# Performance work log

Measured on AMD Instinct MI355X. Metric: run time of the kernel, lower is better.

The kernel has to match this reference:

```python
import jax, jax.numpy as jnp
import numpy as np

NEG_INF = -1000000000.0


def _masked_softmax_scores(a, b, mask):
    # a: [B,H,S,D], b: [B,H,S,D] -> probs [B,H,S,S]
    d = a.shape[-1]
    scores = jnp.einsum('bhqd,bhkd->bhqk', a, b) / jnp.sqrt(jnp.asarray(d, a.dtype))
    scores = jnp.where(mask == 0, jnp.asarray(NEG_INF, scores.dtype), scores)
    return jax.nn.softmax(scores, axis=-1)


def setup_inputs() -> dict:
    key = jax.random.key(0)
    ks = jax.random.split(key, 8)
    B, H, S, D = 8, 12, 512, 64
    return {
        'query': jax.random.normal(ks[0], (B, H, S, D), dtype=jnp.float32),
        'key': jax.random.normal(ks[1], (B, H, S, D), dtype=jnp.float32),
        'value': jax.random.normal(ks[2], (B, H, S, D), dtype=jnp.float32),
        'mask': jax.random.randint(ks[3], (B, 1, S, S), 0, 2, dtype=jnp.int32),
        'x_original1': jax.random.normal(ks[4], (B, H, S, D), dtype=jnp.float32),
        'x_original2': jax.random.normal(ks[5], (B, H, S, D), dtype=jnp.float32),
        'x_position1': jax.random.normal(ks[6], (B, H, S, D), dtype=jnp.float32),
        'x_position2': jax.random.normal(ks[7], (B, H, S, D), dtype=jnp.float32),
    }


def reference(query, key, value, mask, x_original1, x_original2, x_position1, x_position2):
    p_attn = _masked_softmax_scores(query, key, mask)
    p_attn_ww = _masked_softmax_scores(x_original1, x_original2, mask)
    p_attn_wp = _masked_softmax_scores(x_original1, x_position2, mask)
    p_attn_pw = _masked_softmax_scores(x_position1, x_original2, mask)
    p_attn_pp = _masked_softmax_scores(x_position1, x_position2, mask)
    out = jnp.einsum('bhqk,bhkd->bhqd', p_attn, value)
    return (out, p_attn, p_attn_ww, p_attn_wp, p_attn_pw, p_attn_pp)
```

## Files before the change

### kernel.cpp

```cpp
#include <hip/hip_runtime.h>
#include <hip/hip_bf16.h>

typedef _Float16 f16;
typedef f16 f16x2 __attribute__((ext_vector_type(2)));
typedef f16 f16x4 __attribute__((ext_vector_type(4)));
typedef f16 f16x8 __attribute__((ext_vector_type(8)));
typedef float f32x4 __attribute__((ext_vector_type(4)));
typedef float f32x16 __attribute__((ext_vector_type(16)));
typedef int i32x4 __attribute__((ext_vector_type(4)));
typedef unsigned char u8;
typedef u8 u8x4 __attribute__((ext_vector_type(4)));

#define SEQ 512
#define DIM 64
#define NBH 96
#define OUT0 3145728
#define PSZ  25165824
#define MSZ  262144

__device__ __forceinline__ int swz(int row, int colByte) {
    return row * 128 + (colByte ^ ((row & 7) << 4));
}

__global__ __launch_bounds__(256) void scores_softmax(
    const float* __restrict__ q_, const float* __restrict__ k_,
    const float* __restrict__ xo1, const float* __restrict__ xo2,
    const float* __restrict__ xp1, const float* __restrict__ xp2,
    const int* __restrict__ mask, float* __restrict__ dout)
{
    __shared__ __align__(16) f16 As[32 * 64];
    __shared__ __align__(16) f16 Bs[128 * 64];
    __shared__ __align__(16) u8  Ms[32 * 512];
    __shared__ float red[4][32];

    const int tid = threadIdx.x;
    const int bid = blockIdx.x;
    const int b   = bid & 7;
    int t = bid >> 3;
    const int qt = t & 15;
    t >>= 4;
    const int h  = t % 12;
    const int m  = t / 12;
    const int bh = b * 12 + h;

    const float* Ap; const float* Bp;
    if      (m == 0) { Ap = q_;  Bp = k_;  }
    else if (m == 1) { Ap = xo1; Bp = xo2; }
    else if (m == 2) { Ap = xo1; Bp = xp2; }
    else if (m == 3) { Ap = xp1; Bp = xo2; }
    else             { Ap = xp1; Bp = xp2; }

    const int w = tid >> 6, lane = tid & 63, l31 = lane & 31, half = lane >> 5;

    const int* mrow = mask + (size_t)b * MSZ + (size_t)(qt * 32) * SEQ;
#pragma unroll
    for (int i = 0; i < 16; i++) {
        int g = tid + 256 * i;
        i32x4 mv = *reinterpret_cast<const i32x4*>(mrow + g * 4);
        u8x4 pk;
        pk[0] = (u8)(mv[0] != 0); pk[1] = (u8)(mv[1] != 0);
        pk[2] = (u8)(mv[2] != 0); pk[3] = (u8)(mv[3] != 0);
        *reinterpret_cast<u8x4*>(&Ms[g * 4]) = pk;
    }

    const float* Ag = Ap + ((size_t)bh * SEQ + qt * 32) * DIM;
#pragma unroll
    for (int i = 0; i < 2; i++) {
        int g = tid + 256 * i; int row = g >> 4, c4 = g & 15;
        f32x4 v = *reinterpret_cast<const f32x4*>(Ag + row * 64 + c4 * 4);
        f16x4 bb; bb[0]=(f16)v[0]; bb[1]=(f16)v[1]; bb[2]=(f16)v[2]; bb[3]=(f16)v[3];
        *reinterpret_cast<f16x4*>((char*)As + swz(row, c4 * 8)) = bb;
    }
    __syncthreads();

    f16x8 afr[4];
#pragma unroll
    for (int k4 = 0; k4 < 4; k4++)
        afr[k4] = *reinterpret_cast<const f16x8*>((char*)As + swz(l31, k4 * 32 + half * 16));

    f32x16 acc[4];
#pragma unroll
    for (int c = 0; c < 4; c++)
#pragma unroll
        for (int i = 0; i < 16; i++) acc[c][i] = 0.f;

    const float* Bg0 = Bp + (size_t)bh * SEQ * DIM;
    for (int c = 0; c < 4; c++) {
        __syncthreads();
        const float* Bg = Bg0 + (size_t)c * 128 * DIM;
#pragma unroll
        for (int i = 0; i < 8; i++) {
            int g = tid + 256 * i; int row = g >> 4, c4 = g & 15;
            f32x4 v = *reinterpret_cast<const f32x4*>(Bg + row * 64 + c4 * 4);
            f16x4 bb; bb[0]=(f16)v[0]; bb[1]=(f16)v[1]; bb[2]=(f16)v[2]; bb[3]=(f16)v[3];
            *reinterpret_cast<f16x4*>((char*)Bs + swz(row, c4 * 8)) = bb;
        }
        __syncthreads();
        int rb = w * 32 + l31;
#pragma unroll
        for (int k4 = 0; k4 < 4; k4++) {
            f16x8 bfr = *reinterpret_cast<const f16x8*>((char*)Bs + swz(rb, k4 * 32 + half * 16));
            acc[c] = __builtin_amdgcn_mfma_f32_32x32x16_f16(afr[k4], bfr, acc[c], 0, 0, 0);
        }
    }

    float rsum[16];
#pragma unroll
    for (int r = 0; r < 16; r++) rsum[r] = 0.f;
#pragma unroll
    for (int c = 0; c < 4; c++) {
        int kcol = c * 128 + w * 32 + l31;
#pragma unroll
        for (int r = 0; r < 16; r++) {
            int qrow = (r & 3) + 8 * (r >> 2) + 4 * half;
            int mk = Ms[qrow * 512 + kcol];
            float e = mk ? __expf(acc[c][r] * 0.125f) : 0.f;
            acc[c][r] = e;
            rsum[r] += e;
        }
    }
#pragma unroll
    for (int d = 1; d < 32; d <<= 1)
#pragma unroll
        for (int r = 0; r < 16; r++) rsum[r] += __shfl_xor(rsum[r], d);
    if (l31 == 0) {
#pragma unroll
        for (int r = 0; r < 16; r++) {
            int qrow = (r & 3) + 8 * (r >> 2) + 4 * half;
            red[w][qrow] = rsum[r];
        }
    }
    __syncthreads();
    float inv[16];
#pragma unroll
    for (int r = 0; r < 16; r++) {
        int qrow = (r & 3) + 8 * (r >> 2) + 4 * half;
        float s = red[0][qrow] + red[1][qrow] + red[2][qrow] + red[3][qrow];
        inv[r] = 1.0f / s;
    }
    float* P = dout + OUT0 + (size_t)m * PSZ + (size_t)bh * MSZ + (size_t)(qt * 32) * SEQ;
#pragma unroll
    for (int c = 0; c < 4; c++) {
        int kcol = c * 128 + w * 32 + l31;
#pragma unroll
        for (int r = 0; r < 16; r++) {
            int qrow = (r & 3) + 8 * (r >> 2) + 4 * half;
            __builtin_nontemporal_store(acc[c][r] * inv[r], &P[(size_t)qrow * SEQ + kcol]);
        }
    }
}

__global__ __launch_bounds__(256) void vtrans(const float* __restrict__ v, f16* __restrict__ vt)
{
    __shared__ float t[128][65];
    const int tid = threadIdx.x;
    const int bid = blockIdx.x;
    const int b = bid & 7;
    int r = bid >> 3;
    const int ck = r & 3;
    const int h  = r >> 2;
    const int bh = b * 12 + h;
    const float* Vg = v + ((size_t)bh * SEQ + ck * 128) * DIM;
#pragma unroll
    for (int i = 0; i < 8; i++) {
        int g = tid + 256 * i; int row = g >> 4, c4 = g & 15;
        f32x4 vv = *reinterpret_cast<const f32x4*>(Vg + row * 64 + c4 * 4);
        t[row][c4*4+0] = vv[0]; t[row][c4*4+1] = vv[1];
        t[row][c4*4+2] = vv[2]; t[row][c4*4+3] = vv[3];
    }
    __syncthreads();
    f16* Og = vt + (size_t)bh * DIM * SEQ + ck * 128;
#pragma unroll
    for (int i = 0; i < 16; i++) {
        int p = tid + 256 * i; int d = p >> 6; int j = (p & 63) * 2;
        f16x2 o; o[0] = (f16)t[j][d]; o[1] = (f16)t[j + 1][d];
        *reinterpret_cast<f16x2*>(Og + (size_t)d * SEQ + j) = o;
    }
}

__global__ __launch_bounds__(256) void pv_mfma(const float* __restrict__ dout,
                                               const f16* __restrict__ vt,
                                               float* __restrict__ out)
{
    __shared__ __align__(16) f16 Ps[64 * 64];
    __shared__ __align__(16) f16 Vs[64 * 64];
    const int tid = threadIdx.x;
    const int bid = blockIdx.x;
    const int b = bid & 7;
    int r = bid >> 3;
    const int qt = r & 7;
    const int h  = r >> 3;
    const int bh = b * 12 + h;
    const int w = tid >> 6, lane = tid & 63, l31 = lane & 31, half = lane >> 5;
    const int wr = w >> 1, wc = w & 1;

    const float* Pg = dout + OUT0 + (size_t)bh * MSZ + (size_t)(qt * 64) * SEQ;
    const f16* Vg = vt + (size_t)bh * DIM * SEQ;

    f32x16 acc;
#pragma unroll
    for (int i = 0; i < 16; i++) acc[i] = 0.f;

    for (int c = 0; c < 8; c++) {
        __syncthreads();
#pragma unroll
        for (int i = 0; i < 4; i++) {
            int g = tid + 256 * i; int row = g >> 4, c4 = g & 15;
            f32x4 v = __builtin_nontemporal_load(
                reinterpret_cast<const f32x4*>(Pg + (size_t)row * SEQ + c * 64 + c4 * 4));
            f16x4 bb; bb[0]=(f16)v[0]; bb[1]=(f16)v[1]; bb[2]=(f16)v[2]; bb[3]=(f16)v[3];
            *reinterpret_cast<f16x4*>((char*)Ps + swz(row, c4 * 8)) = bb;
        }
#pragma unroll
        for (int i = 0; i < 2; i++) {
            int g = tid + 256 * i; int row = g >> 3, c8 = g & 7;
            f16x8 v = *reinterpret_cast<const f16x8*>(Vg + (size_t)row * SEQ + c * 64 + c8 * 8);
            *reinterpret_cast<f16x8*>((char*)Vs + swz(row, c8 * 16)) = v;
        }
        __syncthreads();
        int qr = wr * 32 + l31, dr = wc * 32 + l31;
#pragma unroll
        for (int k4 = 0; k4 < 4; k4++) {
            int co = k4 * 32 + half * 16;
            f16x8 a  = *reinterpret_cast<const f16x8*>((char*)Ps + swz(qr, co));
            f16x8 bb = *reinterpret_cast<const f16x8*>((char*)Vs + swz(dr, co));
            acc = __builtin_amdgcn_mfma_f32_32x32x16_f16(a, bb, acc, 0, 0, 0);
        }
    }
    float* og = out + ((size_t)bh * SEQ + qt * 64 + wr * 32) * DIM + wc * 32;
#pragma unroll
    for (int r2 = 0; r2 < 16; r2++) {
        int qrow = (r2 & 3) + 8 * (r2 >> 2) + 4 * half;
        og[(size_t)qrow * DIM + l31] = acc[r2];
    }
}

__global__ __launch_bounds__(256) void pv_vec(const float* __restrict__ dout,
                                              const float* __restrict__ v,
                                              float* __restrict__ out)
{
    __shared__ float Vs[128][64];
    const int tid = threadIdx.x;
    const int bid = blockIdx.x;
    const int b = bid & 7;
    int r = bid >> 3;
    const int qt = r & 7;
    const int h  = r >> 3;
    const int bh = b * 12 + h;
    float accv[16];
#pragma unroll
    for (int j = 0; j < 16; j++) accv[j] = 0.f;
    const float* Prow = dout + OUT0 + ((size_t)bh * SEQ + qt * 64 + (tid >> 2)) * SEQ;
    const int dbase = (tid & 3) * 16;
    for (int ck = 0; ck < 4; ck++) {
        __syncthreads();
        const float* Vg = v + ((size_t)bh * SEQ + ck * 128) * DIM;
#pragma unroll
        for (int i = 0; i < 8; i++) {
            int g = tid + 256 * i; int row = g >> 4, c4 = g & 15;
            f32x4 vv = *reinterpret_cast<const f32x4*>(Vg + row * 64 + c4 * 4);
            Vs[row][c4*4+0] = vv[0]; Vs[row][c4*4+1] = vv[1];
            Vs[row][c4*4+2] = vv[2]; Vs[row][c4*4+3] = vv[3];
        }
        __syncthreads();
        for (int kv = 0; kv < 128; kv++) {
            float p = Prow[ck * 128 + kv];
#pragma unroll
            for (int j = 0; j < 16; j++) accv[j] += p * Vs[kv][dbase + j];
        }
    }
    float* og = out + ((size_t)bh * SEQ + qt * 64 + (tid >> 2)) * DIM + dbase;
#pragma unroll
    for (int j = 0; j < 16; j++) og[j] = accv[j];
}

extern "C" void kernel_launch(void* const* d_in, const int* in_sizes, int n_in,
                              void* d_out, int out_size, void* d_ws, size_t ws_size,
                              hipStream_t stream) {
    const float* q_  = (const float*)d_in[0];
    const float* k_  = (const float*)d_in[1];
    const float* v_  = (const float*)d_in[2];
    const int*   msk = (const int*)d_in[3];
    const float* xo1 = (const float*)d_in[4];
    const float* xo2 = (const float*)d_in[5];
    const float* xp1 = (const float*)d_in[6];
    const float* xp2 = (const float*)d_in[7];
    float* out = (float*)d_out;

    scores_softmax<<<5 * NBH * 16, 256, 0, stream>>>(q_, k_, xo1, xo2, xp1, xp2, msk, out);

    const size_t need = (size_t)NBH * DIM * SEQ * sizeof(f16);
    if (ws_size >= need) {
        f16* vt = (f16*)d_ws;
        vtrans<<<NBH * 4, 256, 0, stream>>>(v_, vt);
        pv_mfma<<<NBH * 8, 256, 0, stream>>>(out, vt, out);
    } else {
        pv_vec<<<NBH * 8, 256, 0, stream>>>(out, v_, out);
    }
}
```

Baseline: 688.8 us.

## Fuse five score matrices per block, sharing staged K tiles and mask

Replaces the per-(matrix, 32-row tile) scores kernel with one 512-thread block per (bh, 64-row chunk) that computes all five probability matrices. Each block stages the full B operand (512x64 fp16) in shared memory once and reuses it for both A operands that pair with it (xo2 for xo1/xp1, xp2 for xo1/xp1). The mask tile is converted once and shared across the five outputs. This cuts redundant global reads of B and mask, but uses much more LDS (~107KB) and a smaller grid (768 blocks), which limits occupancy and overlap.

```diff
diff --git a/kernel.cpp b/kernel.cpp
--- a/kernel.cpp
+++ b/kernel.cpp
@@ -22,40 +22,31 @@
     return row * 128 + (colByte ^ ((row & 7) << 4));
 }
 
-__global__ __launch_bounds__(256) void scores_softmax(
+__global__ __launch_bounds__(512, 2) void scores5(
     const float* __restrict__ q_, const float* __restrict__ k_,
     const float* __restrict__ xo1, const float* __restrict__ xo2,
     const float* __restrict__ xp1, const float* __restrict__ xp2,
     const int* __restrict__ mask, float* __restrict__ dout)
 {
-    __shared__ __align__(16) f16 As[32 * 64];
-    __shared__ __align__(16) f16 Bs[128 * 64];
-    __shared__ __align__(16) u8  Ms[32 * 512];
-    __shared__ float red[4][32];
+    __shared__ __align__(16) f16 Bs[SEQ * DIM];
+    __shared__ __align__(16) u8  Ms[64 * SEQ];
+    __shared__ __align__(16) f16 As[3 * 64 * DIM];
+    __shared__ float red[2][4][32];
 
     const int tid = threadIdx.x;
     const int bid = blockIdx.x;
-    const int b   = bid & 7;
-    int t = bid >> 3;
-    const int qt = t & 15;
-    t >>= 4;
-    const int h  = t % 12;
-    const int m  = t / 12;
-    const int bh = b * 12 + h;
-
-    const float* Ap; const float* Bp;
-    if      (m == 0) { Ap = q_;  Bp = k_;  }
-    else if (m == 1) { Ap = xo1; Bp = xo2; }
-    else if (m == 2) { Ap = xo1; Bp = xp2; }
-    else if (m == 3) { Ap = xp1; Bp = xo2; }
-    else             { Ap = xp1; Bp = xp2; }
+    const int qc  = bid / NBH;
+    const int bh  = bid % NBH;
+    const int b   = bh / 12;
 
     const int w = tid >> 6, lane = tid & 63, l31 = lane & 31, half = lane >> 5;
-
-    const int* mrow = mask + (size_t)b * MSZ + (size_t)(qt * 32) * SEQ;
+    const int qsub = w & 1;
+    const int kq   = w >> 1;
+
+    const int* mrow = mask + (size_t)b * MSZ + (size_t)(qc * 64) * SEQ;
 #pragma unroll
     for (int i = 0; i < 16; i++) {
-        int g = tid + 256 * i;
+        int g = tid + 512 * i;
         i32x4 mv = *reinterpret_cast<const i32x4*>(mrow + g * 4);
         u8x4 pk;
         pk[0] = (u8)(mv[0] != 0); pk[1] = (u8)(mv[1] != 0);
@@ -63,91 +54,108 @@
         *reinterpret_cast<u8x4*>(&Ms[g * 4]) = pk;
     }
 
-    const float* Ag = Ap + ((size_t)bh * SEQ + qt * 32) * DIM;
-#pragma unroll
-    for (int i = 0; i < 2; i++) {
-        int g = tid + 256 * i; int row = g >> 4, c4 = g & 15;
-        f32x4 v = *reinterpret_cast<const f32x4*>(Ag + row * 64 + c4 * 4);
-        f16x4 bb; bb[0]=(f16)v[0]; bb[1]=(f16)v[1]; bb[2]=(f16)v[2]; bb[3]=(f16)v[3];
-        *reinterpret_cast<f16x4*>((char*)As + swz(row, c4 * 8)) = bb;
+    {
+        const float* srcs[3] = { q_, xo1, xp1 };
+#pragma unroll
+        for (int s = 0; s < 3; s++) {
+            const float* Ag = srcs[s] + ((size_t)bh * SEQ + qc * 64) * DIM;
+#pragma unroll
+            for (int i = 0; i < 2; i++) {
+                int g = tid + 512 * i; int row = g >> 4, c4 = g & 15;
+                f32x4 v = *reinterpret_cast<const f32x4*>(Ag + row * 64 + c4 * 4);
+                f16x4 hv; hv[0]=(f16)v[0]; hv[1]=(f16)v[1]; hv[2]=(f16)v[2]; hv[3]=(f16)v[3];
+                *reinterpret_cast<f16x4*>((char*)As + s * 8192 + swz(row, c4 * 8)) = hv;
+            }
+        }
     }
     __syncthreads();
 
-    f16x8 afr[4];
-#pragma unroll
-    for (int k4 = 0; k4 < 4; k4++)
-        afr[k4] = *reinterpret_cast<const f16x8*>((char*)As + swz(l31, k4 * 32 + half * 16));
-
-    f32x16 acc[4];
-#pragma unroll
-    for (int c = 0; c < 4; c++)
-#pragma unroll
-        for (int i = 0; i < 16; i++) acc[c][i] = 0.f;
-
-    const float* Bg0 = Bp + (size_t)bh * SEQ * DIM;
-    for (int c = 0; c < 4; c++) {
-        __syncthreads();
-        const float* Bg = Bg0 + (size_t)c * 128 * DIM;
-#pragma unroll
-        for (int i = 0; i < 8; i++) {
-            int g = tid + 256 * i; int row = g >> 4, c4 = g & 15;
-            f32x4 v = *reinterpret_cast<const f32x4*>(Bg + row * 64 + c4 * 4);
-            f16x4 bb; bb[0]=(f16)v[0]; bb[1]=(f16)v[1]; bb[2]=(f16)v[2]; bb[3]=(f16)v[3];
-            *reinterpret_cast<f16x4*>((char*)Bs + swz(row, c4 * 8)) = bb;
-        }
-        __syncthreads();
-        int rb = w * 32 + l31;
-#pragma unroll
-        for (int k4 = 0; k4 < 4; k4++) {
-            f16x8 bfr = *reinterpret_cast<const f16x8*>((char*)Bs + swz(rb, k4 * 32 + half * 16));
-            acc[c] = __builtin_amdgcn_mfma_f32_32x32x16_f16(afr[k4], bfr, acc[c], 0, 0, 0);
-        }
-    }
-
-    float rsum[16];
-#pragma unroll
-    for (int r = 0; r < 16; r++) rsum[r] = 0.f;
-#pragma unroll
-    for (int c = 0; c < 4; c++) {
-        int kcol = c * 128 + w * 32 + l31;
+    f16x8 af0[4], af1[4], af2[4];
+#pragma unroll
+    for (int k4 = 0; k4 < 4; k4++) {
+        af0[k4] = *reinterpret_cast<const f16x8*>((char*)As + 0     + swz(qsub*32 + l31, k4*32 + half*16));
+        af1[k4] = *reinterpret_cast<const f16x8*>((char*)As + 8192  + swz(qsub*32 + l31, k4*32 + half*16));
+        af2[k4] = *reinterpret_cast<const f16x8*>((char*)As + 16384 + swz(qsub*32 + l31, k4*32 + half*16));
+    }
+
+    auto step = [&](const f16x8 (&afr)[4], int mout, const float* bsrc) {
+        if (bsrc) {
+            __syncthreads();
+            const float* Bg = bsrc + (size_t)bh * SEQ * DIM;
+#pragma unroll
+            for (int i = 0; i < 16; i++) {
+                int g = tid + 512 * i; int row = g >> 4, c4 = g & 15;
+                f32x4 v = *reinterpret_cast<const f32x4*>(Bg + row * 64 + c4 * 4);
+                f16x4 hv; hv[0]=(f16)v[0]; hv[1]=(f16)v[1]; hv[2]=(f16)v[2]; hv[3]=(f16)v[3];
+                *reinterpret_cast<f16x4*>((char*)Bs + swz(row, c4 * 8)) = hv;
+            }
+        }
+        __syncthreads();
+
+        f32x16 acc[4];
+#pragma unroll
+        for (int c2 = 0; c2 < 4; c2++) {
+#pragma unroll
+            for (int i = 0; i < 16; i++) acc[c2][i] = 0.f;
+#pragma unroll
+            for (int k4 = 0; k4 < 4; k4++) {
+                f16x8 bf = *reinterpret_cast<const f16x8*>(
+                    (char*)Bs + swz(kq * 128 + c2 * 32 + l31, k4 * 32 + half * 16));
+                acc[c2] = __builtin_amdgcn_mfma_f32_32x32x16_f16(afr[k4], bf, acc[c2], 0, 0, 0);
+            }
+        }
+
+        float rsum[16];
+#pragma unroll
+        for (int r = 0; r < 16; r++) rsum[r] = 0.f;
+#pragma unroll
+        for (int c2 = 0; c2 < 4; c2++) {
+            int kcol = kq * 128 + c2 * 32 + l31;
+#pragma unroll
+            for (int r = 0; r < 16; r++) {
+                int qrow = (r & 3) + 8 * (r >> 2) + 4 * half;
+                float e = Ms[(qsub * 32 + qrow) * SEQ + kcol] ? __expf(acc[c2][r] * 0.125f) : 0.f;
+                acc[c2][r] = e;
+                rsum[r] += e;
+            }
+        }
+#pragma unroll
+        for (int d = 1; d < 32; d <<= 1)
+#pragma unroll
+            for (int r = 0; r < 16; r++) rsum[r] += __shfl_xor(rsum[r], d);
+        if (l31 == 0) {
+#pragma unroll
+            for (int r = 0; r < 16; r++) {
+                int qrow = (r & 3) + 8 * (r >> 2) + 4 * half;
+                red[qsub][kq][qrow] = rsum[r];
+            }
+        }
+        __syncthreads();
+        float inv[16];
 #pragma unroll
         for (int r = 0; r < 16; r++) {
             int qrow = (r & 3) + 8 * (r >> 2) + 4 * half;
-            int mk = Ms[qrow * 512 + kcol];
-            float e = mk ? __expf(acc[c][r] * 0.125f) : 0.f;
-            acc[c][r] = e;
-            rsum[r] += e;
-        }
-    }
-#pragma unroll
-    for (int d = 1; d < 32; d <<= 1)
-#pragma unroll
-        for (int r = 0; r < 16; r++) rsum[r] += __shfl_xor(rsum[r], d);
-    if (l31 == 0) {
-#pragma unroll
-        for (int r = 0; r < 16; r++) {
-            int qrow = (r & 3) + 8 * (r >> 2) + 4 * half;
-            red[w][qrow] = rsum[r];
-        }
-    }
-    __syncthreads();
-    float inv[16];
-#pragma unroll
-    for (int r = 0; r < 16; r++) {
-        int qrow = (r & 3) + 8 * (r >> 2) + 4 * half;
-        float s = red[0][qrow] + red[1][qrow] + red[2][qrow] + red[3][qrow];
-        inv[r] = 1.0f / s;
-    }
-    float* P = dout + OUT0 + (size_t)m * PSZ + (size_t)bh * MSZ + (size_t)(qt * 32) * SEQ;
-#pragma unroll
-    for (int c = 0; c < 4; c++) {
-        int kcol = c * 128 + w * 32 + l31;
-#pragma unroll
-        for (int r = 0; r < 16; r++) {
-            int qrow = (r & 3) + 8 * (r >> 2) + 4 * half;
-            __builtin_nontemporal_store(acc[c][r] * inv[r], &P[(size_t)qrow * SEQ + kcol]);
-        }
-    }
+            inv[r] = 1.0f / (red[qsub][0][qrow] + red[qsub][1][qrow] +
+                             red[qsub][2][qrow] + red[qsub][3][qrow]);
+        }
+        float* P = dout + OUT0 + (size_t)mout * PSZ + (size_t)bh * MSZ + (size_t)(qc * 64) * SEQ;
+#pragma unroll
+        for (int c2 = 0; c2 < 4; c2++) {
+            int kcol = kq * 128 + c2 * 32 + l31;
+#pragma unroll
+            for (int r = 0; r < 16; r++) {
+                int qrow = (r & 3) + 8 * (r >> 2) + 4 * half;
+                __builtin_nontemporal_store(acc[c2][r] * inv[r],
+                                            &P[(size_t)(qsub * 32 + qrow) * SEQ + kcol]);
+            }
+        }
+    };
+
+    step(af0, 0, k_);
+    step(af1, 1, xo2);
+    step(af2, 3, nullptr);
+    step(af1, 2, xp2);
+    step(af2, 4, nullptr);
 }
 
 __global__ __launch_bounds__(256) void vtrans(const float* __restrict__ v, f16* __restrict__ vt)
@@ -287,7 +295,7 @@
     const float* xp2 = (const float*)d_in[7];
     float* out = (float*)d_out;
 
-    scores_softmax<<<5 * NBH * 16, 256, 0, stream>>>(q_, k_, xo1, xo2, xp1, xp2, msk, out);
+    scores5<<<8 * NBH, 512, 0, stream>>>(q_, k_, xo1, xo2, xp1, xp2, msk, out);
 
     const size_t need = (size_t)NBH * DIM * SEQ * sizeof(f16);
     if (ws_size >= need) {
```

Result: faster. 634.7 us (-7.9%).
